# Optimization experiments

Hardware: AMD Instinct MI355X
Metric: run time of the kernel (lower is better)

## Reference

```python
import jax, jax.numpy as jnp
import numpy as np


def setup_inputs() -> dict:
    key = jax.random.key(0)
    ks = jax.random.split(key, 6)
    N, E, F, H, HOP = 100000, 1600000, 128, 128, 3
    x = jax.random.normal(ks[0], (N, F), dtype=jnp.float32)
    edge_index = jax.random.randint(ks[1], (2, E), 0, N, dtype=jnp.int64)
    # per-hop weights, scaled like nn.Linear default init magnitude
    W1 = jax.random.normal(ks[2], (HOP, H, F), dtype=jnp.float32) * (1.0 / np.sqrt(F))
    W2 = jax.random.normal(ks[3], (HOP, H, H), dtype=jnp.float32) * (1.0 / np.sqrt(H))
    W3 = jax.random.normal(ks[4], (HOP, H, H), dtype=jnp.float32) * (1.0 / np.sqrt(H))
    W4 = jax.random.normal(ks[5], (HOP, H, 1), dtype=jnp.float32)
    return {"x": x, "edge_index": edge_index, "W1": W1, "W2": W2, "W3": W3, "W4": W4}


def reference(x, edge_index, W1, W2, W3, W4):
    N = x.shape[0]
    E = edge_index.shape[1]
    H = W1.shape[1]
    hop = W1.shape[0]
    row, col = edge_index[0], edge_index[1]
    edge_attr = jnp.ones((E, 1), dtype=x.dtype)  # as in original forward
    h = jnp.zeros((N, H), dtype=x.dtype)  # initial node_embedding
    for i in range(hop):
        node_feat = x @ W1[i].T                                   # [N,H]
        # gather neighbor embeddings then scatter-sum to destination nodes
        nbr_agg = jax.ops.segment_sum(h[col], row, num_segments=N)  # [N,H]
        edge_emb = jax.nn.relu(edge_attr @ W4[i].T)               # [E,H]
        edge_agg = jax.ops.segment_sum(edge_emb, row, num_segments=N)  # [N,H]
        h = jax.nn.relu(node_feat + nbr_agg @ W2[i].T + edge_agg @ W3[i].T)
        # dropout is identity in eval mode
    return h
```

## Files before the change

kernel.cpp:

```cpp
#include <hip/hip_runtime.h>

#define H 128
#define BCAP 18432

typedef __attribute__((ext_vector_type(8))) short bf16x8;
typedef __attribute__((ext_vector_type(4))) float f32x4;
typedef unsigned int uint;
typedef unsigned short ushort;

__device__ __forceinline__ ushort f2bf(float f) {
    uint u = __builtin_bit_cast(uint, f);
    uint r = u + 0x7FFFu + ((u >> 16) & 1u);
    return (ushort)(r >> 16);
}
__device__ __forceinline__ float bf_lo(uint u) {
    return __builtin_bit_cast(float, u << 16);
}
__device__ __forceinline__ float bf_hi(uint u) {
    return __builtin_bit_cast(float, u & 0xFFFF0000u);
}


__global__ void scatter_direct(const int* __restrict__ ei, int E, int NB,
                               int* __restrict__ gcnt, int2* __restrict__ ebuf) {
    __shared__ int cnt[1024];
    __shared__ int base[1024];
    int blk = blockIdx.x, t = threadIdx.x;
    for (int b = t; b < NB; b += 256) cnt[b] = 0;
    __syncthreads();
    int lo = blk << 12, hi = min(lo + 4096, E);
    for (int e = lo + t; e < hi; e += 256) atomicAdd(&cnt[ei[e] >> 10], 1);
    __syncthreads();
    for (int b = t; b < NB; b += 256) {
        int c = cnt[b];
        base[b] = c ? atomicAdd(&gcnt[b * 16], c) : 0;
        cnt[b] = 0;
    }
    __syncthreads();
    for (int e = lo + t; e < hi; e += 256) {
        int r = ei[e], c = ei[E + e];
        int b = r >> 10;
        int pos = base[b] + atomicAdd(&cnt[b], 1);
        if (pos < BCAP) ebuf[(size_t)b * BCAP + pos] = make_int2(r, c);
    }
}

__global__ __launch_bounds__(1024)
void bucket_csr2(const int2* __restrict__ ebuf, const int* __restrict__ gcnt,
                 int NB, int N, int* __restrict__ deg, int* __restrict__ off,
                 int* __restrict__ colss) {
    __shared__ int rcnt[1024], rloff[1024];
    int b = blockIdx.x, t = threadIdx.x;
    int rowbase = b << 10;
    int ebase = b * BCAP;
    int ne = min(gcnt[b * 16], BCAP);
    rcnt[t] = 0;
    __syncthreads();
    for (int e = t; e < ne; e += 1024) atomicAdd(&rcnt[ebuf[(size_t)ebase + e].x - rowbase], 1);
    __syncthreads();
    int v = rcnt[t];
    rloff[t] = v;
    __syncthreads();
    for (int d = 1; d < 1024; d <<= 1) {
        int u = (t >= d) ? rloff[t - d] : 0;
        __syncthreads();
        rloff[t] += u;
        __syncthreads();
    }
    int ex = rloff[t] - v;
    int row = rowbase + t;
    if (row < N) {
        deg[row] = v;
        off[row] = ebase + ex;
    }
    __syncthreads();
    rloff[t] = ex;
    rcnt[t] = 0;
    __syncthreads();
    for (int e = t; e < ne; e += 1024) {
        int2 rc = ebuf[(size_t)ebase + e];
        int lr = rc.x - rowbase;
        int pz = atomicAdd(&rcnt[lr], 1);
        colss[ebase + rloff[lr] + pz] = rc.y;
    }
}

__global__ void cvec_kernel(const float* __restrict__ W3, const float* __restrict__ W4,
                            float* __restrict__ cvec) {
    int i = blockIdx.x, k = threadIdx.x;
    const float* w3 = W3 + i * H * H + k * H;
    const float* w4 = W4 + i * H;
    float s = 0.f;
    for (int j = 0; j < H; ++j) s += w3[j] * fmaxf(w4[j], 0.f);
    cvec[i * H + k] = s;
}

__global__ void cast_bf16(const float* __restrict__ in, ushort* __restrict__ outp, int n8) {
    int i = blockIdx.x * blockDim.x + threadIdx.x;
    if (i >= n8) return;
    const float4* in4 = (const float4*)in;
    float4 a = in4[2 * i], b = in4[2 * i + 1];
    uint4 o;
    o.x = (uint)f2bf(a.x) | ((uint)f2bf(a.y) << 16);
    o.y = (uint)f2bf(a.z) | ((uint)f2bf(a.w) << 16);
    o.z = (uint)f2bf(b.x) | ((uint)f2bf(b.y) << 16);
    o.w = (uint)f2bf(b.z) | ((uint)f2bf(b.w) << 16);
    ((uint4*)outp)[i] = o;
}


template<int RELU, int OUT_BF16, int CAST0>
__global__ __launch_bounds__(256)
void gemm_pairs(const void* __restrict__ A0, const ushort* __restrict__ W0,
                const ushort* __restrict__ A1, const ushort* __restrict__ W1p,
                int npairs, const int* __restrict__ deg, const float* __restrict__ cvec,
                void* __restrict__ Cout, ushort* __restrict__ xbout, int N)
{
    __shared__ uint4 A4[1024];
    __shared__ uint4 W4[1024];
    int t = threadIdx.x;
    int w = t >> 6, l = t & 63;
    int lg = l >> 4, lr = l & 15;
    int rowBase = blockIdx.x * 128;

    f32x4 acc[2][8];
#pragma unroll
    for (int rt = 0; rt < 2; ++rt)
#pragma unroll
        for (int ct = 0; ct < 8; ++ct) acc[rt][ct] = (f32x4){0.f, 0.f, 0.f, 0.f};

    uint4 ar[4], wr[4];
    int nc = npairs * 2;

    auto stage = [&](int c) {
        int pr = c >> 1, kc = c & 1;
        const uint4* Ag = (const uint4*)(pr ? (const void*)A1 : A0);
        const uint4* Wg = (const uint4*)(pr ? W1p : W0);
#pragma unroll
        for (int it = 0; it < 4; ++it) {
            int idx = it * 256 + t;
            int r = idx >> 3, s = idx & 7;
            int gr = rowBase + r;
            uint4 v = make_uint4(0, 0, 0, 0);
            if (CAST0 && pr == 0) {
                if (gr < N) {
                    const float4* xg = (const float4*)A0;
                    float4 a = xg[(size_t)gr * 32 + (kc * 8 + s) * 2];
                    float4 b = xg[(size_t)gr * 32 + (kc * 8 + s) * 2 + 1];
                    v.x = (uint)f2bf(a.x) | ((uint)f2bf(a.y) << 16);
                    v.y = (uint)f2bf(a.z) | ((uint)f2bf(a.w) << 16);
                    v.z = (uint)f2bf(b.x) | ((uint)f2bf(b.y) << 16);
                    v.w = (uint)f2bf(b.z) | ((uint)f2bf(b.w) << 16);
                    ((uint4*)xbout)[(size_t)gr * 16 + kc * 8 + s] = v;
                }
            } else {
                if (gr < N) v = Ag[(size_t)gr * 16 + kc * 8 + s];
            }
            ar[it] = v;
            wr[it] = Wg[r * 16 + kc * 8 + s];
        }
    };
    auto commit = [&]() {
#pragma unroll
        for (int it = 0; it < 4; ++it) {
            int idx = it * 256 + t;
            int r = idx >> 3, s = idx & 7;
            A4[r * 8 + (s ^ (r & 7))] = ar[it];
            W4[r * 8 + (s ^ (r & 7))] = wr[it];
        }
    };

    stage(0);
    commit();
    __syncthreads();

    for (int c = 0; c < nc; ++c) {
        if (c + 1 < nc) stage(c + 1);
#pragma unroll
        for (int kk = 0; kk < 2; ++kk) {
            int slot = kk * 4 + lg;
            bf16x8 af[2], bfr[8];
#pragma unroll
            for (int rt = 0; rt < 2; ++rt) {
                int r = w * 32 + rt * 16 + lr;
                af[rt] = *(const bf16x8*)&A4[r * 8 + (slot ^ (r & 7))];
            }
#pragma unroll
            for (int ct = 0; ct < 8; ++ct) {
                int r = ct * 16 + lr;
                bfr[ct] = *(const bf16x8*)&W4[r * 8 + (slot ^ (r & 7))];
            }
#pragma unroll
            for (int rt = 0; rt < 2; ++rt)
#pragma unroll
                for (int ct = 0; ct < 8; ++ct)
                    acc[rt][ct] = __builtin_amdgcn_mfma_f32_16x16x32_bf16(
                        af[rt], bfr[ct], acc[rt][ct], 0, 0, 0);
        }
        __syncthreads();
        if (c + 1 < nc) {
            commit();
            __syncthreads();
        }
    }

    float cv[8];
#pragma unroll
    for (int ct = 0; ct < 8; ++ct) cv[ct] = cvec[ct * 16 + lr];
#pragma unroll
    for (int rt = 0; rt < 2; ++rt) {
#pragma unroll
        for (int j = 0; j < 4; ++j) {
            int gr = rowBase + w * 32 + rt * 16 + lg * 4 + j;
            if (gr < N) {
                float d = (float)deg[gr];
#pragma unroll
                for (int ct = 0; ct < 8; ++ct) {
                    int gc = ct * 16 + lr;
                    float v = acc[rt][ct][j] + d * cv[ct];
                    if (RELU) v = fmaxf(v, 0.f);
                    if (OUT_BF16) ((ushort*)Cout)[(size_t)gr * H + gc] = f2bf(v);
                    else ((float*)Cout)[(size_t)gr * H + gc] = v;
                }
            }
        }
    }
}


__global__ void aggregate_sum(const ushort* __restrict__ hsrc,
                              const int* __restrict__ off, const int* __restrict__ deg,
                              const int* __restrict__ cols,
                              ushort* __restrict__ sdst, int N)
{
    int node = blockIdx.x * 4 + (threadIdx.x >> 6);
    if (node >= N) return;
    int l = threadIdx.x & 63;
    int s = off[node], e = s + deg[node];
    const uint* pu = (const uint*)hsrc;
    float ax = 0.f, ay = 0.f;
    int i = s;
    for (; i + 8 <= e; i += 8) {
        uint v0 = pu[(size_t)cols[i]     * 64 + l];
        uint v1 = pu[(size_t)cols[i + 1] * 64 + l];
        uint v2 = pu[(size_t)cols[i + 2] * 64 + l];
        uint v3 = pu[(size_t)cols[i + 3] * 64 + l];
        uint v4 = pu[(size_t)cols[i + 4] * 64 + l];
        uint v5 = pu[(size_t)cols[i + 5] * 64 + l];
        uint v6 = pu[(size_t)cols[i + 6] * 64 + l];
        uint v7 = pu[(size_t)cols[i + 7] * 64 + l];
        ax += bf_lo(v0) + bf_lo(v1) + bf_lo(v2) + bf_lo(v3)
            + bf_lo(v4) + bf_lo(v5) + bf_lo(v6) + bf_lo(v7);
        ay += bf_hi(v0) + bf_hi(v1) + bf_hi(v2) + bf_hi(v3)
            + bf_hi(v4) + bf_hi(v5) + bf_hi(v6) + bf_hi(v7);
    }
    for (; i + 4 <= e; i += 4) {
        uint v0 = pu[(size_t)cols[i]     * 64 + l];
        uint v1 = pu[(size_t)cols[i + 1] * 64 + l];
        uint v2 = pu[(size_t)cols[i + 2] * 64 + l];
        uint v3 = pu[(size_t)cols[i + 3] * 64 + l];
        ax += bf_lo(v0) + bf_lo(v1) + bf_lo(v2) + bf_lo(v3);
        ay += bf_hi(v0) + bf_hi(v1) + bf_hi(v2) + bf_hi(v3);
    }
    for (; i < e; ++i) {
        uint v = pu[(size_t)cols[i] * 64 + l];
        ax += bf_lo(v);
        ay += bf_hi(v);
    }
    ((uint*)sdst)[(size_t)node * 64 + l] = (uint)f2bf(ax) | ((uint)f2bf(ay) << 16);
}


extern "C" void kernel_launch(void* const* d_in, const int* in_sizes, int n_in,
                              void* d_out, int out_size, void* d_ws, size_t ws_size,
                              hipStream_t stream)
{
    const float* x  = (const float*)d_in[0];
    const int*   ei = (const int*)d_in[1];
    const float* W1 = (const float*)d_in[2];
    const float* W2 = (const float*)d_in[3];
    const float* W3 = (const float*)d_in[4];
    const float* W4 = (const float*)d_in[5];
    int N   = in_sizes[0] / H;
    int E   = in_sizes[1] / 2;
    int HOP = in_sizes[2] / (H * H);

    int NB   = (N + 1023) >> 10;
    int NBLK = (E + 4095) >> 12;

    char* ws = (char*)d_ws;
    int*   gcnt  = (int*)ws;
    int*   deg   = gcnt + NB * 16;
    int*   off   = deg + N;
    int*   colss = off + N;
    float* cvec  = (float*)(colss + (size_t)NB * BCAP);
    size_t fo = (((size_t)((char*)(cvec + HOP * H) - ws)) + 255) & ~(size_t)255;
    int2*  ebuf  = (int2*)(ws + fo);
    ushort* W1b  = (ushort*)(ebuf + (size_t)NB * BCAP);
    ushort* W2b  = W1b + (size_t)HOP * H * H;
    ushort* xb   = W2b + (size_t)HOP * H * H;
    ushort* h    = xb + (size_t)N * H;
    ushort* sagg = h + (size_t)N * H;

    hipMemsetAsync(gcnt, 0, sizeof(int) * NB * 16, stream);
    scatter_direct<<<NBLK, 256, 0, stream>>>(ei, E, NB, gcnt, ebuf);
    bucket_csr2<<<NB, 1024, 0, stream>>>(ebuf, gcnt, NB, N, deg, off, colss);

    cvec_kernel<<<HOP, H, 0, stream>>>(W3, W4, cvec);

    int nw8 = HOP * H * H / 8;
    cast_bf16<<<(nw8 + 255) / 256, 256, 0, stream>>>(W1, W1b, nw8);
    cast_bf16<<<(nw8 + 255) / 256, 256, 0, stream>>>(W2, W2b, nw8);

    int gblocks = (N + 127) / 128;
    float* out = (float*)d_out;

    if (HOP == 1) {
        gemm_pairs<1, 0, 1><<<gblocks, 256, 0, stream>>>(x, W1b, nullptr, nullptr, 1,
                                                         deg, cvec, out, xb, N);
        return;
    }
    gemm_pairs<1, 1, 1><<<gblocks, 256, 0, stream>>>(x, W1b, nullptr, nullptr, 1,
                                                     deg, cvec, h, xb, N);

    for (int i = 1; i < HOP; ++i) {
        int last = (i == HOP - 1);
        aggregate_sum<<<(N + 3) / 4, 256, 0, stream>>>(h, off, deg, colss, sagg, N);
        if (last)
            gemm_pairs<1, 0, 0><<<gblocks, 256, 0, stream>>>(xb, W1b + (size_t)i * H * H,
                                                             sagg, W2b + (size_t)i * H * H,
                                                             2, deg, cvec + i * H, out,
                                                             nullptr, N);
        else
            gemm_pairs<1, 1, 0><<<gblocks, 256, 0, stream>>>(xb, W1b + (size_t)i * H * H,
                                                             sagg, W2b + (size_t)i * H * H,
                                                             2, deg, cvec + i * H, h,
                                                             nullptr, N);
    }
}
```

Baseline: 286.0 us.

## Enlarge GEMM tile to 256 rows with 512 threads, drop register prefetch, fuse weight casts

The GEMM kernel now uses 512 threads and 256-row blocks, so each block's loaded weight tile is shared across twice as many rows. The register-staged double-buffer prefetch is replaced by a simple load, sync, compute loop. The two weight-cast launches are merged into one kernel. This halves weight reloads per row and lowers register pressure, but global loads no longer overlap with the MFMA work and there are half as many blocks.

```diff
diff --git a/kernel.cpp b/kernel.cpp
--- a/kernel.cpp
+++ b/kernel.cpp
@@ -95,11 +95,13 @@
     cvec[i * H + k] = s;
 }
 
-__global__ void cast_bf16(const float* __restrict__ in, ushort* __restrict__ outp, int n8) {
+__global__ void cast_w(const float* __restrict__ W1, const float* __restrict__ W2,
+                       ushort* __restrict__ outp, int n8) {
     int i = blockIdx.x * blockDim.x + threadIdx.x;
-    if (i >= n8) return;
-    const float4* in4 = (const float4*)in;
-    float4 a = in4[2 * i], b = in4[2 * i + 1];
+    if (i >= 2 * n8) return;
+    const float4* in4 = (const float4*)((i < n8) ? W1 : W2);
+    int j = (i < n8) ? i : i - n8;
+    float4 a = in4[2 * j], b = in4[2 * j + 1];
     uint4 o;
     o.x = (uint)f2bf(a.x) | ((uint)f2bf(a.y) << 16);
     o.y = (uint)f2bf(a.z) | ((uint)f2bf(a.w) << 16);
@@ -110,18 +112,18 @@
 
 
 template<int RELU, int OUT_BF16, int CAST0>
-__global__ __launch_bounds__(256)
+__global__ __launch_bounds__(512)
 void gemm_pairs(const void* __restrict__ A0, const ushort* __restrict__ W0,
                 const ushort* __restrict__ A1, const ushort* __restrict__ W1p,
                 int npairs, const int* __restrict__ deg, const float* __restrict__ cvec,
                 void* __restrict__ Cout, ushort* __restrict__ xbout, int N)
 {
-    __shared__ uint4 A4[1024];
+    __shared__ uint4 A4[2048];
     __shared__ uint4 W4[1024];
     int t = threadIdx.x;
     int w = t >> 6, l = t & 63;
     int lg = l >> 4, lr = l & 15;
-    int rowBase = blockIdx.x * 128;
+    int rowBase = blockIdx.x * 256;
 
     f32x4 acc[2][8];
 #pragma unroll
@@ -129,78 +131,61 @@
 #pragma unroll
         for (int ct = 0; ct < 8; ++ct) acc[rt][ct] = (f32x4){0.f, 0.f, 0.f, 0.f};
 
-    uint4 ar[4], wr[4];
-    int nc = npairs * 2;
-
-    auto stage = [&](int c) {
-        int pr = c >> 1, kc = c & 1;
+    for (int pr = 0; pr < npairs; ++pr) {
         const uint4* Ag = (const uint4*)(pr ? (const void*)A1 : A0);
         const uint4* Wg = (const uint4*)(pr ? W1p : W0);
-#pragma unroll
-        for (int it = 0; it < 4; ++it) {
-            int idx = it * 256 + t;
-            int r = idx >> 3, s = idx & 7;
-            int gr = rowBase + r;
-            uint4 v = make_uint4(0, 0, 0, 0);
-            if (CAST0 && pr == 0) {
-                if (gr < N) {
-                    const float4* xg = (const float4*)A0;
-                    float4 a = xg[(size_t)gr * 32 + (kc * 8 + s) * 2];
-                    float4 b = xg[(size_t)gr * 32 + (kc * 8 + s) * 2 + 1];
-                    v.x = (uint)f2bf(a.x) | ((uint)f2bf(a.y) << 16);
-                    v.y = (uint)f2bf(a.z) | ((uint)f2bf(a.w) << 16);
-                    v.z = (uint)f2bf(b.x) | ((uint)f2bf(b.y) << 16);
-                    v.w = (uint)f2bf(b.z) | ((uint)f2bf(b.w) << 16);
-                    ((uint4*)xbout)[(size_t)gr * 16 + kc * 8 + s] = v;
+        for (int kc = 0; kc < 2; ++kc) {
+            if (pr || kc) __syncthreads();
+#pragma unroll
+            for (int it = 0; it < 4; ++it) {
+                int idx = it * 512 + t;
+                int r = idx >> 3, s = idx & 7;
+                int gr = rowBase + r;
+                uint4 v = make_uint4(0, 0, 0, 0);
+                if (CAST0 && pr == 0) {
+                    if (gr < N) {
+                        const float4* xg = (const float4*)A0;
+                        float4 a = xg[(size_t)gr * 32 + (kc * 8 + s) * 2];
+                        float4 b = xg[(size_t)gr * 32 + (kc * 8 + s) * 2 + 1];
+                        v.x = (uint)f2bf(a.x) | ((uint)f2bf(a.y) << 16);
+                        v.y = (uint)f2bf(a.z) | ((uint)f2bf(a.w) << 16);
+                        v.z = (uint)f2bf(b.x) | ((uint)f2bf(b.y) << 16);
+                        v.w = (uint)f2bf(b.z) | ((uint)f2bf(b.w) << 16);
+                        ((uint4*)xbout)[(size_t)gr * 16 + kc * 8 + s] = v;
+                    }
+                } else {
+                    if (gr < N) v = Ag[(size_t)gr * 16 + kc * 8 + s];
                 }
-            } else {
-                if (gr < N) v = Ag[(size_t)gr * 16 + kc * 8 + s];
+                A4[r * 8 + (s ^ (r & 7))] = v;
             }
-            ar[it] = v;
-            wr[it] = Wg[r * 16 + kc * 8 + s];
-        }
-    };
-    auto commit = [&]() {
-#pragma unroll
-        for (int it = 0; it < 4; ++it) {
-            int idx = it * 256 + t;
-            int r = idx >> 3, s = idx & 7;
-            A4[r * 8 + (s ^ (r & 7))] = ar[it];
-            W4[r * 8 + (s ^ (r & 7))] = wr[it];
-        }
-    };
-
-    stage(0);
-    commit();
-    __syncthreads();
-
-    for (int c = 0; c < nc; ++c) {
-        if (c + 1 < nc) stage(c + 1);
-#pragma unroll
-        for (int kk = 0; kk < 2; ++kk) {
-            int slot = kk * 4 + lg;
-            bf16x8 af[2], bfr[8];
-#pragma unroll
-            for (int rt = 0; rt < 2; ++rt) {
-                int r = w * 32 + rt * 16 + lr;
-                af[rt] = *(const bf16x8*)&A4[r * 8 + (slot ^ (r & 7))];
+#pragma unroll
+            for (int it = 0; it < 2; ++it) {
+                int idx = it * 512 + t;
+                int r = idx >> 3, s = idx & 7;
+                W4[r * 8 + (s ^ (r & 7))] = Wg[r * 16 + kc * 8 + s];
             }
-#pragma unroll
-            for (int ct = 0; ct < 8; ++ct) {
-                int r = ct * 16 + lr;
-                bfr[ct] = *(const bf16x8*)&W4[r * 8 + (slot ^ (r & 7))];
+            __syncthreads();
+#pragma unroll
+            for (int kk = 0; kk < 2; ++kk) {
+                int slot = kk * 4 + lg;
+                bf16x8 af[2], bfr[8];
+#pragma unroll
+                for (int rt = 0; rt < 2; ++rt) {
+                    int r = w * 32 + rt * 16 + lr;
+                    af[rt] = *(const bf16x8*)&A4[r * 8 + (slot ^ (r & 7))];
+                }
+#pragma unroll
+                for (int ct = 0; ct < 8; ++ct) {
+                    int r = ct * 16 + lr;
+                    bfr[ct] = *(const bf16x8*)&W4[r * 8 + (slot ^ (r & 7))];
+                }
+#pragma unroll
+                for (int rt = 0; rt < 2; ++rt)
+#pragma unroll
+                    for (int ct = 0; ct < 8; ++ct)
+                        acc[rt][ct] = __builtin_amdgcn_mfma_f32_16x16x32_bf16(
+                            af[rt], bfr[ct], acc[rt][ct], 0, 0, 0);
             }
-#pragma unroll
-            for (int rt = 0; rt < 2; ++rt)
-#pragma unroll
-                for (int ct = 0; ct < 8; ++ct)
-                    acc[rt][ct] = __builtin_amdgcn_mfma_f32_16x16x32_bf16(
-                        af[rt], bfr[ct], acc[rt][ct], 0, 0, 0);
-        }
-        __syncthreads();
-        if (c + 1 < nc) {
-            commit();
-            __syncthreads();
         }
     }
 
@@ -309,30 +294,29 @@
     cvec_kernel<<<HOP, H, 0, stream>>>(W3, W4, cvec);
 
     int nw8 = HOP * H * H / 8;
-    cast_bf16<<<(nw8 + 255) / 256, 256, 0, stream>>>(W1, W1b, nw8);
-    cast_bf16<<<(nw8 + 255) / 256, 256, 0, stream>>>(W2, W2b, nw8);
-
-    int gblocks = (N + 127) / 128;
+    cast_w<<<(2 * nw8 + 255) / 256, 256, 0, stream>>>(W1, W2, W1b, nw8);
+
+    int gblocks = (N + 255) / 256;
     float* out = (float*)d_out;
 
     if (HOP == 1) {
-        gemm_pairs<1, 0, 1><<<gblocks, 256, 0, stream>>>(x, W1b, nullptr, nullptr, 1,
+        gemm_pairs<1, 0, 1><<<gblocks, 512, 0, stream>>>(x, W1b, nullptr, nullptr, 1,
                                                          deg, cvec, out, xb, N);
         return;
     }
-    gemm_pairs<1, 1, 1><<<gblocks, 256, 0, stream>>>(x, W1b, nullptr, nullptr, 1,
+    gemm_pairs<1, 1, 1><<<gblocks, 512, 0, stream>>>(x, W1b, nullptr, nullptr, 1,
                                                      deg, cvec, h, xb, N);
 
     for (int i = 1; i < HOP; ++i) {
         int last = (i == HOP - 1);
         aggregate_sum<<<(N + 3) / 4, 256, 0, stream>>>(h, off, deg, colss, sagg, N);
         if (last)
-            gemm_pairs<1, 0, 0><<<gblocks, 256, 0, stream>>>(xb, W1b + (size_t)i * H * H,
+            gemm_pairs<1, 0, 0><<<gblocks, 512, 0, stream>>>(xb, W1b + (size_t)i * H * H,
                                                              sagg, W2b + (size_t)i * H * H,
                                                              2, deg, cvec + i * H, out,
                                                              nullptr, N);
         else
-            gemm_pairs<1, 1, 0><<<gblocks, 256, 0, stream>>>(xb, W1b + (size_t)i * H * H,
+            gemm_pairs<1, 1, 0><<<gblocks, 512, 0, stream>>>(xb, W1b + (size_t)i * H * H,
                                                              sagg, W2b + (size_t)i * H * H,
                                                              2, deg, cvec + i * H, h,
                                                              nullptr, N);
```

Measured after the change: 254.0 us. 1.13x faster.
